# Optimization experiments

Hardware: AMD Instinct MI355X
Metric: run time of the kernel (lower is better)

Reference implementation:

```python
import jax, jax.numpy as jnp
import numpy as np

B, S, DIN, DQ, DK, NGL = 4, 8192, 512, 512, 512, 64


def setup_inputs() -> dict:
    key = jax.random.key(0)
    ks = jax.random.split(key, 10)
    q = jax.random.normal(ks[0], (B, S, DIN), dtype=jnp.float32)
    k = jax.random.normal(ks[1], (B, S, DIN), dtype=jnp.float32)
    v = jax.random.normal(ks[2], (B, S, DIN), dtype=jnp.float32)
    sc_in = 1.0 / np.sqrt(DIN)
    Wq = jax.random.normal(ks[3], (DQ, DIN), dtype=jnp.float32) * sc_in
    bq = jax.random.normal(ks[4], (DQ,), dtype=jnp.float32) * 0.01
    Wk = jax.random.normal(ks[5], (DK, DIN), dtype=jnp.float32) * sc_in
    bk = jax.random.normal(ks[6], (DK,), dtype=jnp.float32) * 0.01
    Wv = jax.random.normal(ks[7], (DK, DIN), dtype=jnp.float32) * sc_in
    bv = jax.random.normal(ks[8], (DK,), dtype=jnp.float32) * 0.01
    # deterministic stand-in for random.sample(range(DK), NGL): unique indices
    rng = np.random.default_rng(0)
    global_tokens = jnp.asarray(rng.choice(DK, size=NGL, replace=False), dtype=jnp.int32)
    return {"q": q, "k": k, "v": v, "Wq": Wq, "bq": bq, "Wk": Wk, "bk": bk,
            "Wv": Wv, "bv": bv, "global_tokens": global_tokens}


def _make_mask(global_tokens):
    # mask[a, b] = -inf iff a < b and neither a nor b is a global token
    idx = jnp.arange(DK)
    glb = jnp.zeros((DK,), dtype=bool).at[global_tokens].set(True)
    cond = (idx[:, None] < idx[None, :]) & (~glb[:, None]) & (~glb[None, :])
    return jnp.where(cond, -jnp.inf, 0.0).astype(jnp.float32)  # [DQ, DK]


def reference(q, k, v, Wq, bq, Wk, bk, Wv, bv, global_tokens):
    Q = q @ Wq.T + bq            # [B, S, DQ]
    K = k @ Wk.T + bk            # [B, S, DK]
    V = v @ Wv.T + bv            # [B, S, DK]
    # num = Q^T K contracting over the sequence axis -> [B, DQ, DK]
    num = jnp.einsum('bsq,bsk->bqk', Q, K)
    mask = _make_mask(global_tokens)
    denom = jnp.asarray(DK, jnp.float32) ** 0.5
    attn = jax.nn.softmax((num + mask) / denom, axis=-1)  # [B, DQ, DK]
    # attn @ V^T -> [B, DQ, S]
    out = jnp.einsum('bqk,bsk->bqs', attn, V)
    return out
```

## Files before the change

### kernel.cpp

```cpp
#include <hip/hip_runtime.h>
#include <stdint.h>

typedef short short8 __attribute__((ext_vector_type(8)));
typedef short short4v __attribute__((ext_vector_type(4)));
typedef float f32x4 __attribute__((ext_vector_type(4)));
typedef unsigned short ushort_t;

__device__ __forceinline__ unsigned short bf16_rne(float x){
  unsigned int u = __float_as_uint(x);
  return (unsigned short)((u + 0x7FFFu + ((u >> 16) & 1u)) >> 16);
}

__device__ __forceinline__ unsigned cvt_pk(float a, float b){
  unsigned r;
  asm("v_cvt_pk_bf16_f32 %0, %1, %2" : "=v"(r) : "v"(a), "v"(b));
  return r;
}

__device__ __forceinline__ void split4(float a0, float a1, float a2, float a3,
                                       unsigned &h0, unsigned &h1,
                                       unsigned &l0, unsigned &l1){
  h0 = cvt_pk(a0, a1); h1 = cvt_pk(a2, a3);
  float f0 = __uint_as_float(h0 << 16), f1 = __uint_as_float(h0 & 0xFFFF0000u);
  float f2 = __uint_as_float(h1 << 16), f3 = __uint_as_float(h1 & 0xFFFF0000u);
  l0 = cvt_pk(a0 - f0, a1 - f1); l1 = cvt_pk(a2 - f2, a3 - f3);
}
__device__ __forceinline__ uint4 hi8(float4 x, float4 y){
  uint4 h; h.x = cvt_pk(x.x, x.y); h.y = cvt_pk(x.z, x.w);
  h.z = cvt_pk(y.x, y.y); h.w = cvt_pk(y.z, y.w); return h;
}
__device__ __forceinline__ void split8(float4 x, float4 y, uint4 &h, uint4 &l){
  split4(x.x, x.y, x.z, x.w, h.x, h.y, l.x, l.y);
  split4(y.x, y.y, y.z, y.w, h.z, h.w, l.z, l.w);
}
__device__ __forceinline__ short8 comb(short4v a, short4v b){
  short8 r; r[0]=a[0]; r[1]=a[1]; r[2]=a[2]; r[3]=a[3];
  r[4]=b[0]; r[5]=b[1]; r[6]=b[2]; r[7]=b[3]; return r;
}

template<int ABF, int BBF, int NT, int EPI, int OB>
__global__ __launch_bounds__(256, 2) void gemm_bt(
    const void* __restrict__ Av, const void* __restrict__ Bv,
    void* __restrict__ Cv, const float* __restrict__ cvec,
    int N, int K, int lda, int ldb, int ldc,
    long sA, long sB, long sC, long scv)
{
  const int bz = blockIdx.y;
  const int tn = N >> 7;
  const int mt = blockIdx.x / tn, nt = blockIdx.x % tn;
  const int m0 = mt << 7, n0 = nt << 7;

  constexpr int AL = (NT == 3) ? 8192 : 4096;
  __shared__ __align__(16) short Ah[AL];
  __shared__ __align__(16) short Bh2[AL];

  const int t = threadIdx.x;
  const int lane = t & 63, wid = t >> 6;
  const int rowS = t >> 1, kh = t & 1;
  const int wr = wid >> 1, wc = wid & 1;
  const int fr = lane & 15, fg = lane >> 4;

  f32x4 acc[4][4];
  const f32x4 Z = {0.f, 0.f, 0.f, 0.f};
  #pragma unroll
  for (int i = 0; i < 4; i++)
    #pragma unroll
    for (int j = 0; j < 4; j++) acc[i][j] = Z;

  const int wbase = rowS * 32;
  const int sw = (rowS >> 1) & 3;
  const int i0 = wbase + ((((kh << 1) + 0) ^ sw) << 3);
  const int i1 = wbase + ((((kh << 1) + 1) ^ sw) << 3);

  const float*    Afp = (const float*)Av   + sA * bz + (long)(m0 + rowS) * lda + kh * 16;
  const ushort_t* Abp = (const ushort_t*)Av + sA * bz + (long)(m0 + rowS) * lda + kh * 16;
  const float*    Bfp = (const float*)Bv   + sB * bz + (long)(n0 + rowS) * ldb + kh * 16;
  const ushort_t* Bbp = (const ushort_t*)Bv + sB * bz + (long)(n0 + rowS) * ldb + kh * 16;

  float4 a0, a1, a2, a3, b0, b1, b2, b3;
  short8 as0, as1, bs0, bs1;
  if (ABF == 0){
    const float4* pa = (const float4*)(Afp);
    a0 = pa[0]; a1 = pa[1]; a2 = pa[2]; a3 = pa[3];
  } else {
    const short8* pa = (const short8*)(Abp);
    as0 = pa[0]; as1 = pa[1];
  }
  if (BBF == 0){
    const float4* pb = (const float4*)(Bfp);
    b0 = pb[0]; b1 = pb[1]; b2 = pb[2]; b3 = pb[3];
  } else {
    const short8* pb = (const short8*)(Bbp);
    bs0 = pb[0]; bs1 = pb[1];
  }

  for (int k0 = 0; k0 < K; k0 += 32){
    __syncthreads();
    if (ABF == 0){
      if (NT == 3){
        uint4 h0, h1, l0, l1;
        split8(a0, a1, h0, l0); split8(a2, a3, h1, l1);
        *(uint4*)&Ah[i0] = h0; *(uint4*)&Ah[i1] = h1;
        *(uint4*)&Ah[i0 + 4096] = l0; *(uint4*)&Ah[i1 + 4096] = l1;
      } else {
        *(uint4*)&Ah[i0] = hi8(a0, a1); *(uint4*)&Ah[i1] = hi8(a2, a3);
      }
    } else {
      *(short8*)&Ah[i0] = as0; *(short8*)&Ah[i1] = as1;
    }
    if (BBF == 0){
      if (NT == 3){
        uint4 h0, h1, l0, l1;
        split8(b0, b1, h0, l0); split8(b2, b3, h1, l1);
        *(uint4*)&Bh2[i0] = h0; *(uint4*)&Bh2[i1] = h1;
        *(uint4*)&Bh2[i0 + 4096] = l0; *(uint4*)&Bh2[i1 + 4096] = l1;
      } else {
        *(uint4*)&Bh2[i0] = hi8(b0, b1); *(uint4*)&Bh2[i1] = hi8(b2, b3);
      }
    } else {
      *(short8*)&Bh2[i0] = bs0; *(short8*)&Bh2[i1] = bs1;
    }
    __syncthreads();

    {
      const int kn = (k0 + 32 < K) ? (k0 + 32) : k0;
      if (ABF == 0){
        const float4* pa = (const float4*)(Afp + kn);
        a0 = pa[0]; a1 = pa[1]; a2 = pa[2]; a3 = pa[3];
      } else {
        const short8* pa = (const short8*)(Abp + kn);
        as0 = pa[0]; as1 = pa[1];
      }
      if (BBF == 0){
        const float4* pb = (const float4*)(Bfp + kn);
        b0 = pb[0]; b1 = pb[1]; b2 = pb[2]; b3 = pb[3];
      } else {
        const short8* pb = (const short8*)(Bbp + kn);
        bs0 = pb[0]; bs1 = pb[1];
      }
    }

    short8 fa[4], fb[4], fal[4], fbl[4];
    #pragma unroll
    for (int mi = 0; mi < 4; mi++){
      int r = wr * 64 + mi * 16 + fr;
      int idx = r * 32 + ((fg ^ ((r >> 1) & 3)) << 3);
      fa[mi] = *(const short8*)&Ah[idx];
      if (NT == 3) fal[mi] = *(const short8*)&Ah[idx + 4096];
    }
    #pragma unroll
    for (int ni = 0; ni < 4; ni++){
      int r = wc * 64 + ni * 16 + fr;
      int idx = r * 32 + ((fg ^ ((r >> 1) & 3)) << 3);
      fb[ni] = *(const short8*)&Bh2[idx];
      if (NT == 3) fbl[ni] = *(const short8*)&Bh2[idx + 4096];
    }
    #pragma unroll
    for (int mi = 0; mi < 4; mi++)
      #pragma unroll
      for (int ni = 0; ni < 4; ni++){
        acc[mi][ni] = __builtin_amdgcn_mfma_f32_16x16x32_bf16(fa[mi], fb[ni], acc[mi][ni], 0, 0, 0);
        if (NT == 3){
          acc[mi][ni] = __builtin_amdgcn_mfma_f32_16x16x32_bf16(fal[mi], fb[ni],  acc[mi][ni], 0, 0, 0);
          acc[mi][ni] = __builtin_amdgcn_mfma_f32_16x16x32_bf16(fa[mi],  fbl[ni], acc[mi][ni], 0, 0, 0);
        }
      }
  }

  float*    Cf = (float*)Cv    + sC * bz;
  ushort_t* Cb = (ushort_t*)Cv + sC * bz;
  #pragma unroll
  for (int mi = 0; mi < 4; mi++)
    #pragma unroll
    for (int ni = 0; ni < 4; ni++){
      int gr0 = m0 + wr * 64 + mi * 16 + fg * 4;
      int gc  = n0 + wc * 64 + ni * 16 + fr;
      #pragma unroll
      for (int j = 0; j < 4; j++){
        float o = acc[mi][ni][j];
        if (EPI == 1) o += cvec[scv * bz + gr0 + j];
        if (OB == 1) Cb[(long)(gr0 + j) * ldc + gc] = bf16_rne(o);
        else         Cf[(long)(gr0 + j) * ldc + gc] = o;
      }
    }
}

__global__ __launch_bounds__(256, 2) void gemm1_tn(
    const float* __restrict__ q, const float* __restrict__ k,
    float* __restrict__ mtp, float* __restrict__ sqp, float* __restrict__ skp)
{
  const int b = blockIdx.z, sp = blockIdx.y;
  const int mt = blockIdx.x >> 2, nt = blockIdx.x & 3;
  const float* qb = q + (long)b * 8192 * 512;
  const float* kb = k + (long)b * 8192 * 512;

  __shared__ __align__(16) unsigned char As[16384];
  __shared__ __align__(16) unsigned char Bs[16384];

  const int t = threadIdx.x;
  const int lam = t & 31, sg = t >> 5;
  const int lane = t & 63, wid = t >> 6;
  const int wr = wid >> 1, wc = wid & 1;
  const int fr = lane & 15, fg = lane >> 4;

  f32x4 acc[4][4];
  const f32x4 Z = {0.f, 0.f, 0.f, 0.f};
  #pragma unroll
  for (int i = 0; i < 4; i++)
    #pragma unroll
    for (int j = 0; j < 4; j++) acc[i][j] = Z;

  float sumk4[4] = {0.f, 0.f, 0.f, 0.f};
  float sumq4[4] = {0.f, 0.f, 0.f, 0.f};

  int wA[4];
  #pragma unroll
  for (int j = 0; j < 4; j++){
    int c = lam * 4 + j;
    int swc = ((c >> 2) ^ ((c & 3) << 1)) & 7;
    wA[j] = c * 128 + ((sg ^ swc) << 4);
  }

  const float* kbase = kb + (long)(sp * 1024 + sg * 4) * 512 + mt * 128 + lam * 4;
  const float* qbase = qb + (long)(sp * 1024 + sg * 4) * 512 + nt * 128 + lam * 4;

  float4 ka0 = *(const float4*)(kbase);
  float4 ka1 = *(const float4*)(kbase + 512);
  float4 ka2 = *(const float4*)(kbase + 1024);
  float4 ka3 = *(const float4*)(kbase + 1536);
  float4 qa0 = *(const float4*)(qbase);
  float4 qa1 = *(const float4*)(qbase + 512);
  float4 qa2 = *(const float4*)(qbase + 1024);
  float4 qa3 = *(const float4*)(qbase + 1536);

  for (int step = 0; step < 32; ++step){
    __syncthreads();
    #pragma unroll
    for (int j = 0; j < 4; j++){
      float a0 = ((const float*)&ka0)[j], a1 = ((const float*)&ka1)[j];
      float a2 = ((const float*)&ka2)[j], a3 = ((const float*)&ka3)[j];
      sumk4[j] += (a0 + a1) + (a2 + a3);
      unsigned h0, h1, l0, l1;
      split4(a0, a1, a2, a3, h0, h1, l0, l1);
      uint4 w; w.x = h0; w.y = h1; w.z = l0; w.w = l1;
      *(uint4*)(As + wA[j]) = w;
    }
    #pragma unroll
    for (int j = 0; j < 4; j++){
      float a0 = ((const float*)&qa0)[j], a1 = ((const float*)&qa1)[j];
      float a2 = ((const float*)&qa2)[j], a3 = ((const float*)&qa3)[j];
      sumq4[j] += (a0 + a1) + (a2 + a3);
      unsigned h0, h1, l0, l1;
      split4(a0, a1, a2, a3, h0, h1, l0, l1);
      uint4 w; w.x = h0; w.y = h1; w.z = l0; w.w = l1;
      *(uint4*)(Bs + wA[j]) = w;
    }
    __syncthreads();

    {
      const int nstep = (step < 31) ? (step + 1) : step;
      const float* pK = kbase + (long)nstep * 16384;
      const float* pQ = qbase + (long)nstep * 16384;
      ka0 = *(const float4*)(pK);
      ka1 = *(const float4*)(pK + 512);
      ka2 = *(const float4*)(pK + 1024);
      ka3 = *(const float4*)(pK + 1536);
      qa0 = *(const float4*)(pQ);
      qa1 = *(const float4*)(pQ + 512);
      qa2 = *(const float4*)(pQ + 1024);
      qa3 = *(const float4*)(pQ + 1536);
    }

    short8 fa[4], fal[4], fb[4], fbl[4];
    #pragma unroll
    for (int mi = 0; mi < 4; mi++){
      int r = wr * 64 + mi * 16 + fr;
      int swc = ((r >> 2) ^ ((r & 3) << 1)) & 7;
      const unsigned char* bp = As + r * 128;
      int u0 = (((fg << 1) + 0) ^ swc) << 4;
      int u1 = (((fg << 1) + 1) ^ swc) << 4;
      fa[mi]  = comb(*(const short4v*)(bp + u0),     *(const short4v*)(bp + u1));
      fal[mi] = comb(*(const short4v*)(bp + u0 + 8), *(const short4v*)(bp + u1 + 8));
    }
    #pragma unroll
    for (int ni = 0; ni < 4; ni++){
      int r = wc * 64 + ni * 16 + fr;
      int swc = ((r >> 2) ^ ((r & 3) << 1)) & 7;
      const unsigned char* bp = Bs + r * 128;
      int u0 = (((fg << 1) + 0) ^ swc) << 4;
      int u1 = (((fg << 1) + 1) ^ swc) << 4;
      fb[ni]  = comb(*(const short4v*)(bp + u0),     *(const short4v*)(bp + u1));
      fbl[ni] = comb(*(const short4v*)(bp + u0 + 8), *(const short4v*)(bp + u1 + 8));
    }
    #pragma unroll
    for (int mi = 0; mi < 4; mi++)
      #pragma unroll
      for (int ni = 0; ni < 4; ni++){
        acc[mi][ni] = __builtin_amdgcn_mfma_f32_16x16x32_bf16(fa[mi],  fb[ni],  acc[mi][ni], 0, 0, 0);
        acc[mi][ni] = __builtin_amdgcn_mfma_f32_16x16x32_bf16(fal[mi], fb[ni],  acc[mi][ni], 0, 0, 0);
        acc[mi][ni] = __builtin_amdgcn_mfma_f32_16x16x32_bf16(fa[mi],  fbl[ni], acc[mi][ni], 0, 0, 0);
      }
  }

  float* Cp = mtp + ((long)sp * 4 + b) * (512 * 512);
  #pragma unroll
  for (int mi = 0; mi < 4; mi++)
    #pragma unroll
    for (int ni = 0; ni < 4; ni++){
      int gr0 = mt * 128 + wr * 64 + mi * 16 + fg * 4;
      int gc  = nt * 128 + wc * 64 + ni * 16 + fr;
      #pragma unroll
      for (int j = 0; j < 4; j++)
        Cp[(long)(gr0 + j) * 512 + gc] = acc[mi][ni][j];
    }

  __syncthreads();
  float* red = (float*)As;
  if (mt == 0){
    #pragma unroll
    for (int j = 0; j < 4; j++) red[sg * 128 + lam * 4 + j] = sumq4[j];
    __syncthreads();
    if (t < 128){
      float s = 0.f;
      #pragma unroll
      for (int g = 0; g < 8; g++) s += red[g * 128 + t];
      sqp[((long)b * 8 + sp) * 512 + nt * 128 + t] = s;
    }
    __syncthreads();
  }
  if (nt == 0){
    #pragma unroll
    for (int j = 0; j < 4; j++) red[sg * 128 + lam * 4 + j] = sumk4[j];
    __syncthreads();
    if (t < 128){
      float s = 0.f;
      #pragma unroll
      for (int g = 0; g < 8; g++) s += red[g * 128 + t];
      skp[((long)b * 8 + sp) * 512 + mt * 128 + t] = s;
    }
  }
}

__global__ __launch_bounds__(256) void reduceM(const float* __restrict__ p, float* __restrict__ o){
  const long i = ((long)blockIdx.x * 256 + threadIdx.x) * 4;
  float4 s = {0.f, 0.f, 0.f, 0.f};
  #pragma unroll
  for (int j = 0; j < 8; j++){
    float4 v = *(const float4*)(p + (long)j * 1048576 + i);
    s.x += v.x; s.y += v.y; s.z += v.z; s.w += v.w;
  }
  *(float4*)(o + i) = s;
}

__global__ __launch_bounds__(256) void transpose512(const float* __restrict__ in, float* __restrict__ outp){
  __shared__ float tile[32][33];
  const int bx = blockIdx.x & 15, by = blockIdx.x >> 4;
  const int tx = threadIdx.x & 31, ty = threadIdx.x >> 5;
  #pragma unroll
  for (int r = 0; r < 4; r++)
    tile[ty + 8*r][tx] = in[(long)(by*32 + ty + 8*r) * 512 + bx*32 + tx];
  __syncthreads();
  #pragma unroll
  for (int r = 0; r < 4; r++)
    outp[(long)(bx*32 + ty + 8*r) * 512 + by*32 + tx] = tile[tx][ty + 8*r];
}

__global__ __launch_bounds__(256) void smallprep(
    const float* __restrict__ sqp, const float* __restrict__ skp,
    const float* __restrict__ Wq, const float* __restrict__ Wk,
    float* __restrict__ wqsq, float* __restrict__ wksk)
{
  const int bid = blockIdx.x;
  const int tau = bid >> 4;
  const int b = (bid >> 2) & 3, ab = bid & 3;
  const float* P = tau ? skp : sqp;
  const float* W = tau ? Wk : Wq;
  float* O = tau ? wksk : wqsq;
  __shared__ float sv[512];
  const int t = threadIdx.x;
  for (int i = t; i < 512; i += 256){
    float s = 0.f;
    #pragma unroll
    for (int g = 0; g < 8; g++) s += P[((long)b * 8 + g) * 512 + i];
    sv[i] = s;
  }
  __syncthreads();
  const int a = ab * 128 + (t >> 1), half = t & 1;
  const float* Wr = W + (long)a * 512 + half * 256;
  const float* sp2 = sv + half * 256;
  float d = 0.f;
  #pragma unroll 8
  for (int j = 0; j < 256; j++) d += Wr[j] * sp2[j];
  d += __shfl_xor(d, 1);
  if (!half) O[(long)b * 512 + a] = d;
}

__global__ __launch_bounds__(256) void softmax_k(
    const float* __restrict__ num, float* __restrict__ attn, float* __restrict__ cv,
    const float* __restrict__ wqsq, const float* __restrict__ wksk,
    const float* __restrict__ bq, const float* __restrict__ bk,
    const float* __restrict__ bv, const int* __restrict__ gt)
{
  const int a = blockIdx.x, b = blockIdx.y;
  const int t = threadIdx.x;
  const int lane = t & 63, wid = t >> 6;
  __shared__ unsigned char gf[512];
  __shared__ float red[4];
  gf[t] = 0; gf[t + 256] = 0;
  __syncthreads();
  if (t < 64) gf[gt[t]] = 1;
  __syncthreads();

  const float* row = num + ((long)b * 512 + a) * 512;
  const float bqa = bq[a], wqa = wqsq[b * 512 + a];
  const int ga = gf[a];
  const int c0 = t, c1 = t + 256;
  float l0 = (row[c0] + wqa * bk[c0] + bqa * wksk[b*512 + c0] + 8192.0f * bqa * bk[c0]) * 0.04419417382415922f;
  float l1 = (row[c1] + wqa * bk[c1] + bqa * wksk[b*512 + c1] + 8192.0f * bqa * bk[c1]) * 0.04419417382415922f;
  if (a < c0 && !ga && !gf[c0]) l0 = -1e30f;
  if (a < c1 && !ga && !gf[c1]) l1 = -1e30f;

  float m = fmaxf(l0, l1);
  #pragma unroll
  for (int o = 32; o; o >>= 1) m = fmaxf(m, __shfl_xor(m, o));
  if (lane == 0) red[wid] = m;
  __syncthreads();
  m = fmaxf(fmaxf(red[0], red[1]), fmaxf(red[2], red[3]));
  __syncthreads();

  float e0 = __expf(l0 - m), e1 = __expf(l1 - m);
  float s = e0 + e1;
  #pragma unroll
  for (int o = 32; o; o >>= 1) s += __shfl_xor(s, o);
  if (lane == 0) red[wid] = s;
  __syncthreads();
  s = red[0] + red[1] + red[2] + red[3];
  __syncthreads();
  const float inv = 1.0f / s;
  const float a0 = e0 * inv, a1 = e1 * inv;
  float* arow = attn + ((long)b * 512 + a) * 512;
  arow[c0] = a0; arow[c1] = a1;

  float cp = a0 * bv[c0] + a1 * bv[c1];
  #pragma unroll
  for (int o = 32; o; o >>= 1) cp += __shfl_xor(cp, o);
  if (lane == 0) red[wid] = cp;
  __syncthreads();
  if (t == 0) cv[(long)b * 512 + a] = red[0] + red[1] + red[2] + red[3];
}

extern "C" void kernel_launch(void* const* d_in, const int* in_sizes, int n_in,
                              void* d_out, int out_size, void* d_ws, size_t ws_size,
                              hipStream_t stream) {
  const float* q  = (const float*)d_in[0];
  const float* k  = (const float*)d_in[1];
  const float* v  = (const float*)d_in[2];
  const float* Wq = (const float*)d_in[3];
  const float* bq = (const float*)d_in[4];
  const float* Wk = (const float*)d_in[5];
  const float* bk = (const float*)d_in[6];
  const float* Wv = (const float*)d_in[7];
  const float* bv = (const float*)d_in[8];
  const int*   gt = (const int*)d_in[9];
  float* out = (float*)d_out;

  float* w = (float*)d_ws;
  float* mtp  = w;
  float* mt   = mtp  + 8388608;
  float* t1   = mt   + 1048576;
  float* numb = t1   + 1048576;
  float* attn = numb + 1048576;
  float* a2b  = attn + 1048576;
  float* wvT  = a2b  + 1048576;
  float* sqp  = wvT  + 262144;
  float* skp  = sqp  + 16384;
  float* wqsq = skp  + 16384;
  float* wksk = wqsq + 2048;
  float* cv   = wksk + 2048;
  ushort_t* a2h = (ushort_t*)a2b;

  transpose512<<<256, 256, 0, stream>>>(Wv, wvT);
  gemm1_tn<<<dim3(16, 8, 4), 256, 0, stream>>>(q, k, mtp, sqp, skp);
  reduceM<<<1024, 256, 0, stream>>>(mtp, mt);
  smallprep<<<32, 256, 0, stream>>>(sqp, skp, Wq, Wk, wqsq, wksk);
  gemm_bt<0,0,3,0,0><<<dim3(16, 4), 256, 0, stream>>>(Wq, mt, t1, nullptr,
      512, 512, 512, 512, 512, 0L, 262144L, 262144L, 0L);
  gemm_bt<0,0,3,0,0><<<dim3(16, 4), 256, 0, stream>>>(t1, Wk, numb, nullptr,
      512, 512, 512, 512, 512, 262144L, 0L, 262144L, 0L);
  softmax_k<<<dim3(512, 4), 256, 0, stream>>>(numb, attn, cv, wqsq, wksk, bq, bk, bv, gt);
  gemm_bt<0,0,1,0,1><<<dim3(16, 4), 256, 0, stream>>>(attn, wvT, a2h, nullptr,
      512, 512, 512, 512, 512, 262144L, 0L, 262144L, 0L);
  gemm_bt<1,0,1,1,0><<<dim3(256, 4), 256, 0, stream>>>(a2h, v, out, cv,
      8192, 512, 512, 512, 8192, 262144L, 4194304L, 4194304L, 512L);
}
```

Baseline: 233.8 us.

## Use 64-tile small GEMMs and more sequence splits for Q^T K partials

Templates the small 512x512 GEMMs on tile size and launches them with 64x64 tiles, giving 256 blocks instead of 64 so more CUs have work. When the workspace is large enough, the first Q^T K reduction over the sequence is split 16 ways instead of 8, with launch bounds raised to 4 blocks per SM. The partial sums are reduced in place, and the workspace layout is compacted to match. In exchange, smaller tiles reuse less data per load, and the extra splits mean more partial-sum traffic in the reduction.

```diff
diff --git a/kernel.cpp b/kernel.cpp
--- a/kernel.cpp
+++ b/kernel.cpp
@@ -10,13 +10,11 @@
   unsigned int u = __float_as_uint(x);
   return (unsigned short)((u + 0x7FFFu + ((u >> 16) & 1u)) >> 16);
 }
-
 __device__ __forceinline__ unsigned cvt_pk(float a, float b){
   unsigned r;
   asm("v_cvt_pk_bf16_f32 %0, %1, %2" : "=v"(r) : "v"(a), "v"(b));
   return r;
 }
-
 __device__ __forceinline__ void split4(float a0, float a1, float a2, float a3,
                                        unsigned &h0, unsigned &h1,
                                        unsigned &l0, unsigned &l1){
@@ -38,127 +36,129 @@
   r[4]=b[0]; r[5]=b[1]; r[6]=b[2]; r[7]=b[3]; return r;
 }
 
-template<int ABF, int BBF, int NT, int EPI, int OB>
+template<int TS, int ABF, int BBF, int NT, int EPI, int OB>
 __global__ __launch_bounds__(256, 2) void gemm_bt(
     const void* __restrict__ Av, const void* __restrict__ Bv,
     void* __restrict__ Cv, const float* __restrict__ cvec,
-    int N, int K, int lda, int ldb, int ldc,
+    int tn, int K, int lda, int ldb, int ldc,
     long sA, long sB, long sC, long scv)
 {
   const int bz = blockIdx.y;
-  const int tn = N >> 7;
   const int mt = blockIdx.x / tn, nt = blockIdx.x % tn;
-  const int m0 = mt << 7, n0 = nt << 7;
-
-  constexpr int AL = (NT == 3) ? 8192 : 4096;
+  const int m0 = mt * TS, n0 = nt * TS;
+
+  constexpr int MI   = TS / 64;
+  constexpr int ROWE = TS * 32;
+  constexpr int AL   = (NT == 3) ? 2 * ROWE : ROWE;
+  constexpr int EL   = (TS == 128) ? 16 : 8;
   __shared__ __align__(16) short Ah[AL];
   __shared__ __align__(16) short Bh2[AL];
 
   const int t = threadIdx.x;
   const int lane = t & 63, wid = t >> 6;
-  const int rowS = t >> 1, kh = t & 1;
+  const int rowS = (TS == 128) ? (t >> 1) : (t >> 2);
+  const int kh   = (TS == 128) ? (t & 1)  : (t & 3);
   const int wr = wid >> 1, wc = wid & 1;
   const int fr = lane & 15, fg = lane >> 4;
 
-  f32x4 acc[4][4];
+  f32x4 acc[2*MI][2*MI];
   const f32x4 Z = {0.f, 0.f, 0.f, 0.f};
   #pragma unroll
-  for (int i = 0; i < 4; i++)
-    #pragma unroll
-    for (int j = 0; j < 4; j++) acc[i][j] = Z;
+  for (int i = 0; i < 2*MI; i++)
+    #pragma unroll
+    for (int j = 0; j < 2*MI; j++) acc[i][j] = Z;
 
   const int wbase = rowS * 32;
   const int sw = (rowS >> 1) & 3;
-  const int i0 = wbase + ((((kh << 1) + 0) ^ sw) << 3);
-  const int i1 = wbase + ((((kh << 1) + 1) ^ sw) << 3);
-
-  const float*    Afp = (const float*)Av   + sA * bz + (long)(m0 + rowS) * lda + kh * 16;
-  const ushort_t* Abp = (const ushort_t*)Av + sA * bz + (long)(m0 + rowS) * lda + kh * 16;
-  const float*    Bfp = (const float*)Bv   + sB * bz + (long)(n0 + rowS) * ldb + kh * 16;
-  const ushort_t* Bbp = (const ushort_t*)Bv + sB * bz + (long)(n0 + rowS) * ldb + kh * 16;
+  const int i0 = wbase + ((((TS == 128) ? (kh << 1) : kh) ^ sw) << 3);
+  const int i1 = (TS == 128) ? (wbase + ((((kh << 1) + 1) ^ sw) << 3)) : 0;
+
+  const float*    Afp = (const float*)Av    + sA * bz + (long)(m0 + rowS) * lda + kh * EL;
+  const ushort_t* Abp = (const ushort_t*)Av + sA * bz + (long)(m0 + rowS) * lda + kh * EL;
+  const float*    Bfp = (const float*)Bv    + sB * bz + (long)(n0 + rowS) * ldb + kh * EL;
+  const ushort_t* Bbp = (const ushort_t*)Bv + sB * bz + (long)(n0 + rowS) * ldb + kh * EL;
 
   float4 a0, a1, a2, a3, b0, b1, b2, b3;
   short8 as0, as1, bs0, bs1;
-  if (ABF == 0){
-    const float4* pa = (const float4*)(Afp);
-    a0 = pa[0]; a1 = pa[1]; a2 = pa[2]; a3 = pa[3];
-  } else {
-    const short8* pa = (const short8*)(Abp);
-    as0 = pa[0]; as1 = pa[1];
-  }
-  if (BBF == 0){
-    const float4* pb = (const float4*)(Bfp);
-    b0 = pb[0]; b1 = pb[1]; b2 = pb[2]; b3 = pb[3];
-  } else {
-    const short8* pb = (const short8*)(Bbp);
-    bs0 = pb[0]; bs1 = pb[1];
-  }
+
+  auto loadAB = [&](int kk){
+    if (ABF == 0){
+      const float4* pa = (const float4*)(Afp + kk);
+      a0 = pa[0]; a1 = pa[1];
+      if (TS == 128){ a2 = pa[2]; a3 = pa[3]; }
+    } else {
+      const short8* pa = (const short8*)(Abp + kk);
+      as0 = pa[0]; if (TS == 128) as1 = pa[1];
+    }
+    if (BBF == 0){
+      const float4* pb = (const float4*)(Bfp + kk);
+      b0 = pb[0]; b1 = pb[1];
+      if (TS == 128){ b2 = pb[2]; b3 = pb[3]; }
+    } else {
+      const short8* pb = (const short8*)(Bbp + kk);
+      bs0 = pb[0]; if (TS == 128) bs1 = pb[1];
+    }
+  };
+
+  loadAB(0);
 
   for (int k0 = 0; k0 < K; k0 += 32){
     __syncthreads();
     if (ABF == 0){
       if (NT == 3){
-        uint4 h0, h1, l0, l1;
-        split8(a0, a1, h0, l0); split8(a2, a3, h1, l1);
-        *(uint4*)&Ah[i0] = h0; *(uint4*)&Ah[i1] = h1;
-        *(uint4*)&Ah[i0 + 4096] = l0; *(uint4*)&Ah[i1 + 4096] = l1;
+        uint4 h0, l0; split8(a0, a1, h0, l0);
+        *(uint4*)&Ah[i0] = h0; *(uint4*)&Ah[i0 + ROWE] = l0;
+        if (TS == 128){
+          uint4 h1, l1; split8(a2, a3, h1, l1);
+          *(uint4*)&Ah[i1] = h1; *(uint4*)&Ah[i1 + ROWE] = l1;
+        }
       } else {
-        *(uint4*)&Ah[i0] = hi8(a0, a1); *(uint4*)&Ah[i1] = hi8(a2, a3);
+        *(uint4*)&Ah[i0] = hi8(a0, a1);
+        if (TS == 128) *(uint4*)&Ah[i1] = hi8(a2, a3);
       }
     } else {
-      *(short8*)&Ah[i0] = as0; *(short8*)&Ah[i1] = as1;
+      *(short8*)&Ah[i0] = as0;
+      if (TS == 128) *(short8*)&Ah[i1] = as1;
     }
     if (BBF == 0){
       if (NT == 3){
-        uint4 h0, h1, l0, l1;
-        split8(b0, b1, h0, l0); split8(b2, b3, h1, l1);
-        *(uint4*)&Bh2[i0] = h0; *(uint4*)&Bh2[i1] = h1;
-        *(uint4*)&Bh2[i0 + 4096] = l0; *(uint4*)&Bh2[i1 + 4096] = l1;
+        uint4 h0, l0; split8(b0, b1, h0, l0);
+        *(uint4*)&Bh2[i0] = h0; *(uint4*)&Bh2[i0 + ROWE] = l0;
+        if (TS == 128){
+          uint4 h1, l1; split8(b2, b3, h1, l1);
+          *(uint4*)&Bh2[i1] = h1; *(uint4*)&Bh2[i1 + ROWE] = l1;
+        }
       } else {
-        *(uint4*)&Bh2[i0] = hi8(b0, b1); *(uint4*)&Bh2[i1] = hi8(b2, b3);
+        *(uint4*)&Bh2[i0] = hi8(b0, b1);
+        if (TS == 128) *(uint4*)&Bh2[i1] = hi8(b2, b3);
       }
     } else {
-      *(short8*)&Bh2[i0] = bs0; *(short8*)&Bh2[i1] = bs1;
-    }
-    __syncthreads();
-
-    {
-      const int kn = (k0 + 32 < K) ? (k0 + 32) : k0;
-      if (ABF == 0){
-        const float4* pa = (const float4*)(Afp + kn);
-        a0 = pa[0]; a1 = pa[1]; a2 = pa[2]; a3 = pa[3];
-      } else {
-        const short8* pa = (const short8*)(Abp + kn);
-        as0 = pa[0]; as1 = pa[1];
-      }
-      if (BBF == 0){
-        const float4* pb = (const float4*)(Bfp + kn);
-        b0 = pb[0]; b1 = pb[1]; b2 = pb[2]; b3 = pb[3];
-      } else {
-        const short8* pb = (const short8*)(Bbp + kn);
-        bs0 = pb[0]; bs1 = pb[1];
-      }
-    }
-
-    short8 fa[4], fb[4], fal[4], fbl[4];
-    #pragma unroll
-    for (int mi = 0; mi < 4; mi++){
-      int r = wr * 64 + mi * 16 + fr;
+      *(short8*)&Bh2[i0] = bs0;
+      if (TS == 128) *(short8*)&Bh2[i1] = bs1;
+    }
+    __syncthreads();
+
+    loadAB((k0 + 32 < K) ? (k0 + 32) : k0);
+
+    short8 fa[2*MI], fb[2*MI], fal[2*MI], fbl[2*MI];
+    #pragma unroll
+    for (int mi = 0; mi < 2*MI; mi++){
+      int r = wr * (32*MI) + mi * 16 + fr;
       int idx = r * 32 + ((fg ^ ((r >> 1) & 3)) << 3);
       fa[mi] = *(const short8*)&Ah[idx];
-      if (NT == 3) fal[mi] = *(const short8*)&Ah[idx + 4096];
-    }
-    #pragma unroll
-    for (int ni = 0; ni < 4; ni++){
-      int r = wc * 64 + ni * 16 + fr;
+      if (NT == 3) fal[mi] = *(const short8*)&Ah[idx + ROWE];
+    }
+    #pragma unroll
+    for (int ni = 0; ni < 2*MI; ni++){
+      int r = wc * (32*MI) + ni * 16 + fr;
       int idx = r * 32 + ((fg ^ ((r >> 1) & 3)) << 3);
       fb[ni] = *(const short8*)&Bh2[idx];
-      if (NT == 3) fbl[ni] = *(const short8*)&Bh2[idx + 4096];
-    }
-    #pragma unroll
-    for (int mi = 0; mi < 4; mi++)
+      if (NT == 3) fbl[ni] = *(const short8*)&Bh2[idx + ROWE];
+    }
+    #pragma unroll
+    for (int mi = 0; mi < 2*MI; mi++)
       #pragma unroll
-      for (int ni = 0; ni < 4; ni++){
+      for (int ni = 0; ni < 2*MI; ni++){
         acc[mi][ni] = __builtin_amdgcn_mfma_f32_16x16x32_bf16(fa[mi], fb[ni], acc[mi][ni], 0, 0, 0);
         if (NT == 3){
           acc[mi][ni] = __builtin_amdgcn_mfma_f32_16x16x32_bf16(fal[mi], fb[ni],  acc[mi][ni], 0, 0, 0);
@@ -170,11 +170,11 @@
   float*    Cf = (float*)Cv    + sC * bz;
   ushort_t* Cb = (ushort_t*)Cv + sC * bz;
   #pragma unroll
-  for (int mi = 0; mi < 4; mi++)
-    #pragma unroll
-    for (int ni = 0; ni < 4; ni++){
-      int gr0 = m0 + wr * 64 + mi * 16 + fg * 4;
-      int gc  = n0 + wc * 64 + ni * 16 + fr;
+  for (int mi = 0; mi < 2*MI; mi++)
+    #pragma unroll
+    for (int ni = 0; ni < 2*MI; ni++){
+      int gr0 = m0 + wr * (32*MI) + mi * 16 + fg * 4;
+      int gc  = n0 + wc * (32*MI) + ni * 16 + fr;
       #pragma unroll
       for (int j = 0; j < 4; j++){
         float o = acc[mi][ni][j];
@@ -185,10 +185,12 @@
     }
 }
 
-__global__ __launch_bounds__(256, 2) void gemm1_tn(
+template<int NSP>
+__global__ __launch_bounds__(256, 4) void gemm1_tn(
     const float* __restrict__ q, const float* __restrict__ k,
     float* __restrict__ mtp, float* __restrict__ sqp, float* __restrict__ skp)
 {
+  constexpr int STEPS = 256 / NSP;
   const int b = blockIdx.z, sp = blockIdx.y;
   const int mt = blockIdx.x >> 2, nt = blockIdx.x & 3;
   const float* qb = q + (long)b * 8192 * 512;
@@ -221,8 +223,8 @@
     wA[j] = c * 128 + ((sg ^ swc) << 4);
   }
 
-  const float* kbase = kb + (long)(sp * 1024 + sg * 4) * 512 + mt * 128 + lam * 4;
-  const float* qbase = qb + (long)(sp * 1024 + sg * 4) * 512 + nt * 128 + lam * 4;
+  const float* kbase = kb + (long)(sp * (STEPS * 32) + sg * 4) * 512 + mt * 128 + lam * 4;
+  const float* qbase = qb + (long)(sp * (STEPS * 32) + sg * 4) * 512 + nt * 128 + lam * 4;
 
   float4 ka0 = *(const float4*)(kbase);
   float4 ka1 = *(const float4*)(kbase + 512);
@@ -233,7 +235,7 @@
   float4 qa2 = *(const float4*)(qbase + 1024);
   float4 qa3 = *(const float4*)(qbase + 1536);
 
-  for (int step = 0; step < 32; ++step){
+  for (int step = 0; step < STEPS; ++step){
     __syncthreads();
     #pragma unroll
     for (int j = 0; j < 4; j++){
@@ -258,7 +260,7 @@
     __syncthreads();
 
     {
-      const int nstep = (step < 31) ? (step + 1) : step;
+      const int nstep = (step < STEPS - 1) ? (step + 1) : step;
       const float* pK = kbase + (long)nstep * 16384;
       const float* pQ = qbase + (long)nstep * 16384;
       ka0 = *(const float4*)(pK);
@@ -321,10 +323,10 @@
     for (int j = 0; j < 4; j++) red[sg * 128 + lam * 4 + j] = sumq4[j];
     __syncthreads();
     if (t < 128){
-      float s = 0.f;
+      float s2 = 0.f;
       #pragma unroll
-      for (int g = 0; g < 8; g++) s += red[g * 128 + t];
-      sqp[((long)b * 8 + sp) * 512 + nt * 128 + t] = s;
+      for (int gg = 0; gg < 8; gg++) s2 += red[gg * 128 + t];
+      sqp[((long)b * NSP + sp) * 512 + nt * 128 + t] = s2;
     }
     __syncthreads();
   }
@@ -333,23 +335,26 @@
     for (int j = 0; j < 4; j++) red[sg * 128 + lam * 4 + j] = sumk4[j];
     __syncthreads();
     if (t < 128){
-      float s = 0.f;
+      float s2 = 0.f;
       #pragma unroll
-      for (int g = 0; g < 8; g++) s += red[g * 128 + t];
-      skp[((long)b * 8 + sp) * 512 + mt * 128 + t] = s;
-    }
-  }
-}
-
-__global__ __launch_bounds__(256) void reduceM(const float* __restrict__ p, float* __restrict__ o){
-  const long i = ((long)blockIdx.x * 256 + threadIdx.x) * 4;
+      for (int gg = 0; gg < 8; gg++) s2 += red[gg * 128 + t];
+      skp[((long)b * NSP + sp) * 512 + mt * 128 + t] = s2;
+    }
+  }
+}
+
+template<int NS>
+__global__ __launch_bounds__(256) void reduceM(float* __restrict__ p){
+  const int bid = blockIdx.x;
+  const int b = bid >> 8;
+  const long i = (long)(bid & 255) * 1024 + threadIdx.x * 4;
   float4 s = {0.f, 0.f, 0.f, 0.f};
   #pragma unroll
-  for (int j = 0; j < 8; j++){
-    float4 v = *(const float4*)(p + (long)j * 1048576 + i);
+  for (int j = 0; j < NS; j++){
+    float4 v = *(const float4*)(p + ((long)j * 4 + b) * 262144 + i);
     s.x += v.x; s.y += v.y; s.z += v.z; s.w += v.w;
   }
-  *(float4*)(o + i) = s;
+  *(float4*)(p + (long)b * 262144 + i) = s;
 }
 
 __global__ __launch_bounds__(256) void transpose512(const float* __restrict__ in, float* __restrict__ outp){
@@ -368,7 +373,7 @@
 __global__ __launch_bounds__(256) void smallprep(
     const float* __restrict__ sqp, const float* __restrict__ skp,
     const float* __restrict__ Wq, const float* __restrict__ Wk,
-    float* __restrict__ wqsq, float* __restrict__ wksk)
+    float* __restrict__ wqsq, float* __restrict__ wksk, int nsp)
 {
   const int bid = blockIdx.x;
   const int tau = bid >> 4;
@@ -380,8 +385,7 @@
   const int t = threadIdx.x;
   for (int i = t; i < 512; i += 256){
     float s = 0.f;
-    #pragma unroll
-    for (int g = 0; g < 8; g++) s += P[((long)b * 8 + g) * 512 + i];
+    for (int g = 0; g < nsp; g++) s += P[((long)b * nsp + g) * 512 + i];
     sv[i] = s;
   }
   __syncthreads();
@@ -464,32 +468,37 @@
   const int*   gt = (const int*)d_in[9];
   float* out = (float*)d_out;
 
+  const bool big = ws_size >= (size_t)68 * 1024 * 1024;
+  const int NSP = big ? 16 : 8;
+
   float* w = (float*)d_ws;
-  float* mtp  = w;
-  float* mt   = mtp  + 8388608;
-  float* t1   = mt   + 1048576;
-  float* numb = t1   + 1048576;
-  float* attn = numb + 1048576;
-  float* a2b  = attn + 1048576;
-  float* wvT  = a2b  + 1048576;
-  float* sqp  = wvT  + 262144;
-  float* skp  = sqp  + 16384;
-  float* wqsq = skp  + 16384;
-  float* wksk = wqsq + 2048;
-  float* cv   = wksk + 2048;
-  ushort_t* a2h = (ushort_t*)a2b;
-
-  transpose512<<<256, 256, 0, stream>>>(Wv, wvT);
-  gemm1_tn<<<dim3(16, 8, 4), 256, 0, stream>>>(q, k, mtp, sqp, skp);
-  reduceM<<<1024, 256, 0, stream>>>(mtp, mt);
-  smallprep<<<32, 256, 0, stream>>>(sqp, skp, Wq, Wk, wqsq, wksk);
-  gemm_bt<0,0,3,0,0><<<dim3(16, 4), 256, 0, stream>>>(Wq, mt, t1, nullptr,
-      512, 512, 512, 512, 512, 0L, 262144L, 262144L, 0L);
-  gemm_bt<0,0,3,0,0><<<dim3(16, 4), 256, 0, stream>>>(t1, Wk, numb, nullptr,
-      512, 512, 512, 512, 512, 262144L, 0L, 262144L, 0L);
-  softmax_k<<<dim3(512, 4), 256, 0, stream>>>(numb, attn, cv, wqsq, wksk, bq, bk, bv, gt);
-  gemm_bt<0,0,1,0,1><<<dim3(16, 4), 256, 0, stream>>>(attn, wvT, a2h, nullptr,
-      512, 512, 512, 512, 512, 262144L, 0L, 262144L, 0L);
-  gemm_bt<1,0,1,1,0><<<dim3(256, 4), 256, 0, stream>>>(a2h, v, out, cv,
-      8192, 512, 512, 512, 8192, 262144L, 4194304L, 4194304L, 512L);
-}
+  float* MT   = w;
+  float* T1   = w + 1048576;
+  float* NUM  = w + 2097152;
+  float* ATT  = w + 3145728;
+  float* A2H  = w + 4194304;
+  float* WVT  = A2H + 524288;
+  float* SM   = w + (long)NSP * 1048576;
+  float* SQP  = SM;
+  float* SKP  = SQP + 32768;
+  float* WQS  = SKP + 32768;
+  float* WKS  = WQS + 2048;
+  float* CV   = WKS + 2048;
+  ushort_t* a2h = (ushort_t*)A2H;
+
+  if (big) gemm1_tn<16><<<dim3(16, 16, 4), 256, 0, stream>>>(q, k, w, SQP, SKP);
+  else     gemm1_tn<8> <<<dim3(16,  8, 4), 256, 0, stream>>>(q, k, w, SQP, SKP);
+  if (big) reduceM<16><<<1024, 256, 0, stream>>>(w);
+  else     reduceM<8> <<<1024, 256, 0, stream>>>(w);
+  transpose512<<<256, 256, 0, stream>>>(Wv, WVT);
+  smallprep<<<32, 256, 0, stream>>>(SQP, SKP, Wq, Wk, WQS, WKS, NSP);
+  gemm_bt<64,0,0,3,0,0><<<dim3(64, 4), 256, 0, stream>>>(Wq, MT, T1, nullptr,
+      8, 512, 512, 512, 512, 0L, 262144L, 262144L, 0L);
+  gemm_bt<64,0,0,3,0,0><<<dim3(64, 4), 256, 0, stream>>>(T1, Wk, NUM, nullptr,
+      8, 512, 512, 512, 512, 262144L, 0L, 262144L, 0L);
+  softmax_k<<<dim3(512, 4), 256, 0, stream>>>(NUM, ATT, CV, WQS, WKS, bq, bk, bv, gt);
+  gemm_bt<64,0,0,1,0,1><<<dim3(64, 4), 256, 0, stream>>>(ATT, WVT, a2h, nullptr,
+      8, 512, 512, 512, 512, 262144L, 0L, 262144L, 0L);
+  gemm_bt<128,1,0,1,1,0><<<dim3(256, 4), 256, 0, stream>>>(a2h, v, out, CV,
+      64, 512, 512, 512, 8192, 262144L, 4194304L, 4194304L, 512L);
+}
```

Result: slower. 665.4 us (+184.6%).
